# Kernel optimization log

Measured on AMD Instinct MI355X. Metric: run time of the kernel, lower is better.

Reference implementation:

```python
import jax, jax.numpy as jnp
import numpy as np

N_NODES = 100000
N_EDGES = 3200000
N_FEAT = 256
HIDDEN = 64
N_CLASSES = 6


def gcn_conv(x, W, b, src, dst, n_nodes):
    """PyG GCNConv: out = D^{-1/2} (A + I) D^{-1/2} X W + b (self-loops added)."""
    h = x @ W  # [N, out]
    loops = jnp.arange(n_nodes, dtype=src.dtype)
    src2 = jnp.concatenate([src, loops])
    dst2 = jnp.concatenate([dst, loops])
    # degree over destination nodes (edge weight 1), including self-loops
    deg = jax.ops.segment_sum(jnp.ones_like(dst2, dtype=h.dtype), dst2,
                              num_segments=n_nodes)
    dis = jnp.where(deg > 0, jax.lax.rsqrt(deg), 0.0)  # deg^{-1/2}
    norm = dis[src2] * dis[dst2]  # [E+N]
    msg = h[src2] * norm[:, None]  # gather + scale
    out = jax.ops.segment_sum(msg, dst2, num_segments=n_nodes)  # scatter-add
    return out + b


def setup_inputs() -> dict:
    key = jax.random.key(0)
    ks = jax.random.split(key, 5)
    x = jax.random.normal(ks[0], (N_NODES, N_FEAT), dtype=jnp.float32)
    edge_index = jax.random.randint(ks[1], (2, N_EDGES), 0, N_NODES, dtype=jnp.int64)
    W1 = jax.random.normal(ks[2], (N_FEAT, HIDDEN), dtype=jnp.float32) / np.sqrt(N_FEAT)
    b1 = jnp.zeros((HIDDEN,), dtype=jnp.float32)
    W2 = jax.random.normal(ks[3], (HIDDEN, HIDDEN), dtype=jnp.float32) / np.sqrt(HIDDEN)
    b2 = jnp.zeros((HIDDEN,), dtype=jnp.float32)
    Wfc = jax.random.normal(ks[4], (HIDDEN, N_CLASSES), dtype=jnp.float32) / np.sqrt(HIDDEN)
    bfc = jnp.zeros((N_CLASSES,), dtype=jnp.float32)
    return {"x": x, "edge_index": edge_index, "W1": W1, "b1": b1,
            "W2": W2, "b2": b2, "Wfc": Wfc, "bfc": bfc}


def reference(x, edge_index, W1, b1, W2, b2, Wfc, bfc):
    src, dst = edge_index[0], edge_index[1]
    n = x.shape[0]
    h = jax.nn.relu(gcn_conv(x, W1, b1, src, dst, n))
    # dropout(p=0.2) is identity in eval mode
    h = jax.nn.relu(gcn_conv(h, W2, b2, src, dst, n))
    return h @ Wfc + bfc
```

## Files before the change

kernel.cpp:

```cpp
#include <hip/hip_runtime.h>
#include <hip/hip_fp16.h>
#include <math.h>

#define NFEAT 256
#define HID 64
#define NCLS 6
#define NBMX 1600
#define CAPB 4096
#define CHUNK 16384
#define FUSED_LDS 32768

typedef float vf4 __attribute__((ext_vector_type(4)));
typedef int   vi4 __attribute__((ext_vector_type(4)));


__global__ __launch_bounds__(256) void k_count(const int* __restrict__ dst,
                                               int* __restrict__ C, int E, int nbuck) {
  __shared__ int cnt[NBMX];
  int t = threadIdx.x;
  for (int i = t; i < nbuck; i += 256) cnt[i] = 0;
  __syncthreads();
  int e0 = blockIdx.x * CHUNK;
  int e1 = e0 + CHUNK;
  if (e1 > E) e1 = E;
  for (int r0 = e0; r0 < e1; r0 += 1024) {
    int i0 = r0 + t * 4;
    if (i0 + 4 <= e1) {
      vi4 dv = __builtin_nontemporal_load((const vi4*)&dst[i0]);
      atomicAdd(&cnt[dv.x >> 6], 1);
      atomicAdd(&cnt[dv.y >> 6], 1);
      atomicAdd(&cnt[dv.z >> 6], 1);
      atomicAdd(&cnt[dv.w >> 6], 1);
    } else {
      for (int q = 0; q < 4; ++q)
        if (i0 + q < e1) atomicAdd(&cnt[dst[i0 + q] >> 6], 1);
    }
  }
  __syncthreads();
  int* Crow = C + (size_t)blockIdx.x * nbuck;
  for (int i = t; i < nbuck; i += 256) Crow[i] = cnt[i];
}


__global__ __launch_bounds__(256) void k_scan_cols(int* __restrict__ C,
                                                   int* __restrict__ T,
                                                   int nblk, int nbuck) {
  int b = blockIdx.x * 256 + threadIdx.x;
  if (b >= nbuck) return;
  int run = 0;
  int blk = 0;
  for (; blk + 4 <= nblk; blk += 4) {
    int c0 = C[(size_t)(blk + 0) * nbuck + b];
    int c1 = C[(size_t)(blk + 1) * nbuck + b];
    int c2 = C[(size_t)(blk + 2) * nbuck + b];
    int c3 = C[(size_t)(blk + 3) * nbuck + b];
    C[(size_t)(blk + 0) * nbuck + b] = run; run += c0;
    C[(size_t)(blk + 1) * nbuck + b] = run; run += c1;
    C[(size_t)(blk + 2) * nbuck + b] = run; run += c2;
    C[(size_t)(blk + 3) * nbuck + b] = run; run += c3;
  }
  for (; blk < nblk; ++blk) {
    int c = C[(size_t)blk * nbuck + b];
    C[(size_t)blk * nbuck + b] = run;
    run += c;
  }
  T[b] = run;
}


__global__ __launch_bounds__(256) void k_scanb(const int* __restrict__ T,
                                               int* __restrict__ bbase, int nbuck) {
  __shared__ int sh[256];
  __shared__ int carry;
  int t = threadIdx.x;
  if (t == 0) carry = 0;
  __syncthreads();
  for (int base = 0; base < nbuck; base += 256) {
    int v = (base + t < nbuck) ? T[base + t] : 0;
    sh[t] = v;
    __syncthreads();
    for (int off = 1; off < 256; off <<= 1) {
      int x = sh[t];
      int y = (t >= off) ? sh[t - off] : 0;
      __syncthreads();
      sh[t] = x + y;
      __syncthreads();
    }
    if (base + t < nbuck) bbase[base + t] = carry + sh[t] - v;
    __syncthreads();
    if (t == 255) carry += sh[255];
    __syncthreads();
  }
}


__global__ __launch_bounds__(256) void k_fused(const int* __restrict__ src,
                                               const int* __restrict__ dst,
                                               const int* __restrict__ C,
                                               const int* __restrict__ bbase,
                                               unsigned* __restrict__ packed,
                                               int E, int nbuck, int nbb,
                                               const float* __restrict__ X,
                                               const float* __restrict__ W1,
                                               __half* __restrict__ H16, int n) {
  extern __shared__ char smem[];
  int t = threadIdx.x;

  if (blockIdx.x < nbb) {
    int* baseL = (int*)smem;
    int* cnt   = baseL + NBMX;
    const int* Crow = C + (size_t)blockIdx.x * nbuck;
    for (int i = t; i < nbuck; i += 256) {
      baseL[i] = bbase[i] + Crow[i];
      cnt[i] = 0;
    }
    __syncthreads();

    int e0 = blockIdx.x * CHUNK;
    int e1 = e0 + CHUNK;
    if (e1 > E) e1 = E;
    for (int r0 = e0; r0 < e1; r0 += 1024) {
      int i0 = r0 + t * 4;
      int s4[4], d4[4];
      bool full = (i0 + 4 <= e1);
      if (full) {
        vi4 sv = __builtin_nontemporal_load((const vi4*)&src[i0]);
        vi4 dv = __builtin_nontemporal_load((const vi4*)&dst[i0]);
        s4[0] = sv.x; s4[1] = sv.y; s4[2] = sv.z; s4[3] = sv.w;
        d4[0] = dv.x; d4[1] = dv.y; d4[2] = dv.z; d4[3] = dv.w;
      } else {
        for (int q = 0; q < 4; ++q)
          if (i0 + q < e1) { s4[q] = src[i0 + q]; d4[q] = dst[i0 + q]; }
      }
#pragma unroll
      for (int q = 0; q < 4; ++q) {
        if (i0 + q < e1) {
          int b = d4[q] >> 6;
          int slot = atomicAdd(&cnt[b], 1);
          packed[(size_t)baseL[b] + slot] =
              ((unsigned)s4[q] << 6) | (unsigned)(d4[q] & 63);
        }
      }
    }
  } else {
    float* Wl = (float*)smem;
    float* Xl = Wl + 4096;
    const int row0 = (blockIdx.x - nbb) * 64;
    const int tc = t & 15;
    const int tr = t >> 4;
    float acc[4][4] = {};

    for (int k0 = 0; k0 < NFEAT; k0 += 64) {
      __syncthreads();
#pragma unroll
      for (int i = 0; i < 4; ++i) {
        int idx = t * 4 + i * 1024;
        int kr = idx >> 6, c = idx & 63;
        *(vf4*)&Wl[idx] = *(const vf4*)&W1[(size_t)(k0 + kr) * 64 + c];
      }
#pragma unroll
      for (int i = 0; i < 4; ++i) {
        int idx = t * 4 + i * 1024;
        int r = idx >> 6, c = idx & 63;
        int row = row0 + r;
        vf4 v = {0.f, 0.f, 0.f, 0.f};
        if (row < n) v = __builtin_nontemporal_load((const vf4*)&X[(size_t)row * NFEAT + k0 + c]);
        *(vf4*)&Xl[idx] = v;
      }
      __syncthreads();
#pragma unroll 4
      for (int kk = 0; kk < 64; kk += 4) {
        float4 xv[4], wv[4];
#pragma unroll
        for (int r = 0; r < 4; ++r) xv[r] = *(float4*)&Xl[(tr * 4 + r) * 64 + kk];
#pragma unroll
        for (int q = 0; q < 4; ++q) wv[q] = *(float4*)&Wl[(kk + q) * 64 + tc * 4];
#pragma unroll
        for (int r = 0; r < 4; ++r) {
          const float xr[4] = {xv[r].x, xv[r].y, xv[r].z, xv[r].w};
#pragma unroll
          for (int q = 0; q < 4; ++q) {
            acc[r][0] += xr[q] * wv[q].x;
            acc[r][1] += xr[q] * wv[q].y;
            acc[r][2] += xr[q] * wv[q].z;
            acc[r][3] += xr[q] * wv[q].w;
          }
        }
      }
    }
#pragma unroll
    for (int r = 0; r < 4; ++r) {
      int row = row0 + tr * 4 + r;
      if (row < n) {
        __half2 h01 = __floats2half2_rn(acc[r][0], acc[r][1]);
        __half2 h23 = __floats2half2_rn(acc[r][2], acc[r][3]);
        uint2 st;
        st.x = *reinterpret_cast<unsigned*>(&h01);
        st.y = *reinterpret_cast<unsigned*>(&h23);
        ((uint2*)H16)[(size_t)row * 16 + tc] = st;
      }
    }
  }
}


__global__ __launch_bounds__(256) void k_build(unsigned* __restrict__ packed,
                                               const int* __restrict__ T,
                                               const int* __restrict__ bbase,
                                               int2* __restrict__ rowrange,
                                               float* __restrict__ dis,
                                               int n, int nbuck) {
  __shared__ unsigned buf[CAPB];
  __shared__ unsigned outb[CAPB];
  __shared__ int cnt4[4][64];
  __shared__ int cur4[4][64];
  __shared__ int offi[64];
  __shared__ int offx[64];
  __shared__ int cntl[64];
  int b = blockIdx.x;
  int t = threadIdx.x;
  int g = t >> 6;
  int m = T[b];
  if (m > CAPB) m = CAPB;
  int bb = bbase[b];
  unsigned* pb = packed + bb;

  cnt4[g][t & 63] = 0;
  for (int k = t; k < m; k += 256) buf[k] = pb[k];
  __syncthreads();
  for (int k = t; k < m; k += 256) atomicAdd(&cnt4[g][buf[k] & 63u], 1);
  __syncthreads();
  if (t < 64) {
    int c0 = cnt4[0][t], c1 = cnt4[1][t], c2 = cnt4[2][t], c3 = cnt4[3][t];
    int tot = c0 + c1 + c2 + c3;
    cntl[t] = tot;
    offi[t] = tot;
    cur4[0][t] = 0;
    cur4[1][t] = c0;
    cur4[2][t] = c0 + c1;
    cur4[3][t] = c0 + c1 + c2;
  }
  __syncthreads();
  for (int off = 1; off < 64; off <<= 1) {
    int x = (t < 64) ? offi[t] : 0;
    int y = (t >= off && t < 64) ? offi[t - off] : 0;
    __syncthreads();
    if (t < 64) offi[t] = x + y;
    __syncthreads();
  }
  if (t < 64) {
    offx[t] = offi[t] - cntl[t];
    int v = b * 64 + t;
    if (v < n) {
      rowrange[v] = make_int2(bb + offx[t], cntl[t]);
      dis[v] = rsqrtf((float)cntl[t] + 1.0f);
    }
#pragma unroll
    for (int gg = 0; gg < 4; ++gg) cur4[gg][t] += offx[t];
  }
  __syncthreads();
  for (int k = t; k < m; k += 256) {
    unsigned e = buf[k];
    int dl = e & 63u;
    int q = atomicAdd(&cur4[g][dl], 1);
    outb[q] = e >> 6;
  }
  __syncthreads();
  for (int k = t; k < m; k += 256) pb[k] = outb[k];
}


__global__ __launch_bounds__(256) void k_agg_gemm(const int2* __restrict__ rowrange,
                                                  const int* __restrict__ srcs,
                                                  const __half* __restrict__ g16,
                                                  const float* __restrict__ dis,
                                                  const float* __restrict__ b1,
                                                  const float* __restrict__ W2,
                                                  __half* __restrict__ g2out, int n) {
  __shared__ __half2 W2h[64 * 32];
  __shared__ float arow[16][68];
  int t = threadIdx.x;
  for (int i = t; i < 2048; i += 256) {
    float2 f = *(const float2*)&W2[(size_t)i * 2];
    W2h[i] = __floats2half2_rn(f.x, f.y);
  }

  int grp = t >> 4, lane = t & 15;
  int v = blockIdx.x * 16 + grp;
  bool active = (v < n);
  const uint2* g2 = (const uint2*)g16;

  float rx = 0.f, ry = 0.f, rz = 0.f, rw = 0.f;
  if (active) {
    int2 rr = rowrange[v];
    int j = rr.x, end = rr.x + rr.y;
    float dv = dis[v];
    uint2 su = g2[(size_t)v * 16 + lane];
    float2 f0 = __half22float2(*reinterpret_cast<__half2*>(&su.x));
    float2 f1 = __half22float2(*reinterpret_cast<__half2*>(&su.y));
    float ax = dv * f0.x, ay = dv * f0.y, az = dv * f1.x, aw = dv * f1.y;

    for (; j + 8 <= end; j += 8) {
      int s[8];
#pragma unroll
      for (int q = 0; q < 8; ++q) s[q] = __builtin_nontemporal_load(&srcs[j + q]);
      float ds[8];
      uint2 a[8];
#pragma unroll
      for (int q = 0; q < 8; ++q) { ds[q] = dis[s[q]]; a[q] = g2[(size_t)s[q] * 16 + lane]; }
#pragma unroll
      for (int q = 0; q < 8; ++q) {
        float2 p0 = __half22float2(*reinterpret_cast<__half2*>(&a[q].x));
        float2 p1 = __half22float2(*reinterpret_cast<__half2*>(&a[q].y));
        ax = fmaf(ds[q], p0.x, ax); ay = fmaf(ds[q], p0.y, ay);
        az = fmaf(ds[q], p1.x, az); aw = fmaf(ds[q], p1.y, aw);
      }
    }
    for (; j < end; ++j) {
      int s0 = __builtin_nontemporal_load(&srcs[j]);
      float ds = dis[s0];
      uint2 a0 = g2[(size_t)s0 * 16 + lane];
      float2 p0 = __half22float2(*reinterpret_cast<__half2*>(&a0.x));
      float2 p1 = __half22float2(*reinterpret_cast<__half2*>(&a0.y));
      ax = fmaf(ds, p0.x, ax); ay = fmaf(ds, p0.y, ay);
      az = fmaf(ds, p1.x, az); aw = fmaf(ds, p1.y, aw);
    }
    float4 bb = *(const float4*)&b1[lane * 4];
    rx = fmaxf(fmaf(dv, ax, bb.x), 0.f);
    ry = fmaxf(fmaf(dv, ay, bb.y), 0.f);
    rz = fmaxf(fmaf(dv, az, bb.z), 0.f);
    rw = fmaxf(fmaf(dv, aw, bb.w), 0.f);
  }
  arow[grp][lane * 4 + 0] = rx;
  arow[grp][lane * 4 + 1] = ry;
  arow[grp][lane * 4 + 2] = rz;
  arow[grp][lane * 4 + 3] = rw;
  __syncthreads();

  if (active) {
    float o0 = 0.f, o1 = 0.f, o2 = 0.f, o3 = 0.f;
    int c2 = lane * 2;
#pragma unroll 4
    for (int k = 0; k < 64; ++k) {
      float a = arow[grp][k];
      float2 w01 = __half22float2(W2h[k * 32 + c2]);
      float2 w23 = __half22float2(W2h[k * 32 + c2 + 1]);
      o0 = fmaf(a, w01.x, o0);
      o1 = fmaf(a, w01.y, o1);
      o2 = fmaf(a, w23.x, o2);
      o3 = fmaf(a, w23.y, o3);
    }
    float dvv = dis[v];
    __half2 h01 = __floats2half2_rn(o0 * dvv, o1 * dvv);
    __half2 h23 = __floats2half2_rn(o2 * dvv, o3 * dvv);
    uint2 st;
    st.x = *reinterpret_cast<unsigned*>(&h01);
    st.y = *reinterpret_cast<unsigned*>(&h23);
    ((uint2*)g2out)[(size_t)v * 16 + lane] = st;
  }
}


__global__ __launch_bounds__(256) void k_agg_fc(const int2* __restrict__ rowrange,
                                                const int* __restrict__ srcs,
                                                const __half* __restrict__ g16,
                                                const float* __restrict__ dis,
                                                const float* __restrict__ b2,
                                                const float* __restrict__ Wfc,
                                                const float* __restrict__ bfc,
                                                float* __restrict__ outp, int n) {
  __shared__ float Wl[64 * NCLS];
  __shared__ float bl[8];
  int t = threadIdx.x;
  for (int i = t; i < 64 * NCLS; i += 256) Wl[i] = Wfc[i];
  if (t < NCLS) bl[t] = bfc[t];
  __syncthreads();

  int grp = t >> 4, lane = t & 15;
  int v = blockIdx.x * 16 + grp;
  bool active = (v < n);
  const uint2* g2 = (const uint2*)g16;

  float r0 = 0.f, r1 = 0.f, r2 = 0.f, r3 = 0.f;
  if (active) {
    int2 rr = rowrange[v];
    int j = rr.x, end = rr.x + rr.y;
    uint2 su = g2[(size_t)v * 16 + lane];
    float2 f0 = __half22float2(*reinterpret_cast<__half2*>(&su.x));
    float2 f1 = __half22float2(*reinterpret_cast<__half2*>(&su.y));
    float ax = f0.x, ay = f0.y, az = f1.x, aw = f1.y;

    for (; j + 8 <= end; j += 8) {
      int s[8];
#pragma unroll
      for (int q = 0; q < 8; ++q) s[q] = __builtin_nontemporal_load(&srcs[j + q]);
      uint2 a[8];
#pragma unroll
      for (int q = 0; q < 8; ++q) a[q] = g2[(size_t)s[q] * 16 + lane];
#pragma unroll
      for (int q = 0; q < 8; ++q) {
        float2 p0 = __half22float2(*reinterpret_cast<__half2*>(&a[q].x));
        float2 p1 = __half22float2(*reinterpret_cast<__half2*>(&a[q].y));
        ax += p0.x; ay += p0.y; az += p1.x; aw += p1.y;
      }
    }
    for (; j < end; ++j) {
      int s0 = __builtin_nontemporal_load(&srcs[j]);
      uint2 a0 = g2[(size_t)s0 * 16 + lane];
      float2 p0 = __half22float2(*reinterpret_cast<__half2*>(&a0.x));
      float2 p1 = __half22float2(*reinterpret_cast<__half2*>(&a0.y));
      ax += p0.x; ay += p0.y; az += p1.x; aw += p1.y;
    }
    float dv = dis[v];
    float4 bb = *(const float4*)&b2[lane * 4];
    r0 = fmaxf(fmaf(dv, ax, bb.x), 0.f);
    r1 = fmaxf(fmaf(dv, ay, bb.y), 0.f);
    r2 = fmaxf(fmaf(dv, az, bb.z), 0.f);
    r3 = fmaxf(fmaf(dv, aw, bb.w), 0.f);
  }

  float p[NCLS];
#pragma unroll
  for (int jj = 0; jj < NCLS; ++jj) p[jj] = 0.f;
  int k0 = lane * 4;
#pragma unroll
  for (int q = 0; q < 4; ++q) {
    float a = (q == 0) ? r0 : (q == 1) ? r1 : (q == 2) ? r2 : r3;
#pragma unroll
    for (int jj = 0; jj < NCLS; ++jj)
      p[jj] = fmaf(a, Wl[(k0 + q) * NCLS + jj], p[jj]);
  }
#pragma unroll
  for (int m = 1; m < 16; m <<= 1) {
#pragma unroll
    for (int jj = 0; jj < NCLS; ++jj)
      p[jj] += __shfl_xor(p[jj], m, 64);
  }
  if (active && lane < NCLS)
    outp[(size_t)v * NCLS + lane] = p[lane] + bl[lane];
}


extern "C" void kernel_launch(void* const* d_in, const int* in_sizes, int n_in,
                              void* d_out, int out_size, void* d_ws, size_t ws_size,
                              hipStream_t stream) {
  const float* x   = (const float*)d_in[0];
  const int*   ei  = (const int*)d_in[1];
  const float* W1  = (const float*)d_in[2];
  const float* b1  = (const float*)d_in[3];
  const float* W2  = (const float*)d_in[4];
  const float* b2  = (const float*)d_in[5];
  const float* Wfc = (const float*)d_in[6];
  const float* bfc = (const float*)d_in[7];
  float* out = (float*)d_out;

  const int n = in_sizes[0] / NFEAT;
  const int E = in_sizes[1] / 2;
  const int* src = ei;
  const int* dst = ei + E;
  const int nbuck = (n + 63) >> 6;
  const int nbb = (E + CHUNK - 1) / CHUNK;
  const int ntile = (n + 63) / 64;

  char* ws = (char*)d_ws;
  size_t off = 0;
  auto alloc = [&](size_t bytes) -> void* {
    void* p = (void*)(ws + off);
    off += (bytes + 255) & ~(size_t)255;
    return p;
  };
  float* dis      = (float*)alloc((size_t)n * 4);
  int2*  rowrange = (int2*)alloc((size_t)n * 8);
  int*   C        = (int*)alloc((size_t)nbb * nbuck * 4);
  int*   T        = (int*)alloc((size_t)nbuck * 4);
  int*   bbase    = (int*)alloc((size_t)nbuck * 4);
  unsigned* packed = (unsigned*)alloc((size_t)E * 4);
  __half* bufA16  = (__half*)alloc((size_t)n * HID * 2);
  __half* bufC16  = (__half*)alloc((size_t)n * HID * 2);

  k_count<<<nbb, 256, 0, stream>>>(dst, C, E, nbuck);
  k_scan_cols<<<(nbuck + 255) / 256, 256, 0, stream>>>(C, T, nbb, nbuck);
  k_scanb<<<1, 256, 0, stream>>>(T, bbase, nbuck);
  k_fused<<<nbb + ntile, 256, FUSED_LDS, stream>>>(src, dst, C, bbase, packed,
                                                   E, nbuck, nbb, x, W1, bufA16, n);
  k_build<<<nbuck, 256, 0, stream>>>(packed, T, bbase, rowrange, dis, n, nbuck);

  k_agg_gemm<<<(n + 15) / 16, 256, 0, stream>>>(rowrange, (const int*)packed, bufA16,
                                                dis, b1, W2, bufC16, n);

  k_agg_fc<<<(n + 15) / 16, 256, 0, stream>>>(rowrange, (const int*)packed, bufC16,
                                              dis, b2, Wfc, bfc, out, n);
}
```

Before: 288.8 us.

## Prescale layer-1 features by source norm in build; shuffle-based layer-2 GEMM

```diff
diff --git a/kernel.cpp b/kernel.cpp
--- a/kernel.cpp
+++ b/kernel.cpp
@@ -209,6 +209,7 @@
                                                const int* __restrict__ bbase,
                                                int2* __restrict__ rowrange,
                                                float* __restrict__ dis,
+                                               __half* __restrict__ g1,
                                                int n, int nbuck) {
   __shared__ unsigned buf[CAPB];
   __shared__ unsigned outb[CAPB];
@@ -217,6 +218,7 @@
   __shared__ int offi[64];
   __shared__ int offx[64];
   __shared__ int cntl[64];
+  __shared__ float disl[64];
   int b = blockIdx.x;
   int t = threadIdx.x;
   int g = t >> 6;
@@ -250,10 +252,12 @@
   }
   if (t < 64) {
     offx[t] = offi[t] - cntl[t];
+    float dv = rsqrtf((float)cntl[t] + 1.0f);
+    disl[t] = dv;
     int v = b * 64 + t;
     if (v < n) {
       rowrange[v] = make_int2(bb + offx[t], cntl[t]);
-      dis[v] = rsqrtf((float)cntl[t] + 1.0f);
+      dis[v] = dv;
     }
 #pragma unroll
     for (int gg = 0; gg < 4; ++gg) cur4[gg][t] += offx[t];
@@ -267,6 +271,20 @@
   }
   __syncthreads();
   for (int k = t; k < m; k += 256) pb[k] = outb[k];
+
+  __half2* g1h = (__half2*)g1;
+#pragma unroll
+  for (int i = 0; i < 8; ++i) {
+    int idx = t + i * 256;
+    int r = idx >> 5, e = idx & 31;
+    int v = b * 64 + r;
+    if (v < n) {
+      size_t p = (size_t)v * 32 + e;
+      float2 f = __half22float2(g1h[p]);
+      float d = disl[r];
+      g1h[p] = __floats2half2_rn(f.x * d, f.y * d);
+    }
+  }
 }
 
 
@@ -278,86 +296,81 @@
                                                   const float* __restrict__ W2,
                                                   __half* __restrict__ g2out, int n) {
   __shared__ __half2 W2h[64 * 32];
-  __shared__ float arow[16][68];
   int t = threadIdx.x;
   for (int i = t; i < 2048; i += 256) {
     float2 f = *(const float2*)&W2[(size_t)i * 2];
     W2h[i] = __floats2half2_rn(f.x, f.y);
   }
+  __syncthreads();
 
   int grp = t >> 4, lane = t & 15;
   int v = blockIdx.x * 16 + grp;
-  bool active = (v < n);
+  if (v >= n) return;
   const uint2* g2 = (const uint2*)g16;
 
-  float rx = 0.f, ry = 0.f, rz = 0.f, rw = 0.f;
-  if (active) {
-    int2 rr = rowrange[v];
-    int j = rr.x, end = rr.x + rr.y;
-    float dv = dis[v];
-    uint2 su = g2[(size_t)v * 16 + lane];
-    float2 f0 = __half22float2(*reinterpret_cast<__half2*>(&su.x));
-    float2 f1 = __half22float2(*reinterpret_cast<__half2*>(&su.y));
-    float ax = dv * f0.x, ay = dv * f0.y, az = dv * f1.x, aw = dv * f1.y;
-
-    for (; j + 8 <= end; j += 8) {
-      int s[8];
-#pragma unroll
-      for (int q = 0; q < 8; ++q) s[q] = __builtin_nontemporal_load(&srcs[j + q]);
-      float ds[8];
-      uint2 a[8];
-#pragma unroll
-      for (int q = 0; q < 8; ++q) { ds[q] = dis[s[q]]; a[q] = g2[(size_t)s[q] * 16 + lane]; }
-#pragma unroll
-      for (int q = 0; q < 8; ++q) {
-        float2 p0 = __half22float2(*reinterpret_cast<__half2*>(&a[q].x));
-        float2 p1 = __half22float2(*reinterpret_cast<__half2*>(&a[q].y));
-        ax = fmaf(ds[q], p0.x, ax); ay = fmaf(ds[q], p0.y, ay);
-        az = fmaf(ds[q], p1.x, az); aw = fmaf(ds[q], p1.y, aw);
-      }
-    }
-    for (; j < end; ++j) {
-      int s0 = __builtin_nontemporal_load(&srcs[j]);
-      float ds = dis[s0];
-      uint2 a0 = g2[(size_t)s0 * 16 + lane];
-      float2 p0 = __half22float2(*reinterpret_cast<__half2*>(&a0.x));
-      float2 p1 = __half22float2(*reinterpret_cast<__half2*>(&a0.y));
-      ax = fmaf(ds, p0.x, ax); ay = fmaf(ds, p0.y, ay);
-      az = fmaf(ds, p1.x, az); aw = fmaf(ds, p1.y, aw);
-    }
-    float4 bb = *(const float4*)&b1[lane * 4];
-    rx = fmaxf(fmaf(dv, ax, bb.x), 0.f);
-    ry = fmaxf(fmaf(dv, ay, bb.y), 0.f);
-    rz = fmaxf(fmaf(dv, az, bb.z), 0.f);
-    rw = fmaxf(fmaf(dv, aw, bb.w), 0.f);
-  }
-  arow[grp][lane * 4 + 0] = rx;
-  arow[grp][lane * 4 + 1] = ry;
-  arow[grp][lane * 4 + 2] = rz;
-  arow[grp][lane * 4 + 3] = rw;
-  __syncthreads();
-
-  if (active) {
-    float o0 = 0.f, o1 = 0.f, o2 = 0.f, o3 = 0.f;
-    int c2 = lane * 2;
-#pragma unroll 4
-    for (int k = 0; k < 64; ++k) {
-      float a = arow[grp][k];
-      float2 w01 = __half22float2(W2h[k * 32 + c2]);
-      float2 w23 = __half22float2(W2h[k * 32 + c2 + 1]);
-      o0 = fmaf(a, w01.x, o0);
-      o1 = fmaf(a, w01.y, o1);
-      o2 = fmaf(a, w23.x, o2);
-      o3 = fmaf(a, w23.y, o3);
-    }
-    float dvv = dis[v];
-    __half2 h01 = __floats2half2_rn(o0 * dvv, o1 * dvv);
-    __half2 h23 = __floats2half2_rn(o2 * dvv, o3 * dvv);
-    uint2 st;
-    st.x = *reinterpret_cast<unsigned*>(&h01);
-    st.y = *reinterpret_cast<unsigned*>(&h23);
-    ((uint2*)g2out)[(size_t)v * 16 + lane] = st;
-  }
+  int2 rr = rowrange[v];
+  int j = rr.x, end = rr.x + rr.y;
+  uint2 su = g2[(size_t)v * 16 + lane];
+  float2 f0 = __half22float2(*reinterpret_cast<__half2*>(&su.x));
+  float2 f1 = __half22float2(*reinterpret_cast<__half2*>(&su.y));
+  float ax = f0.x, ay = f0.y, az = f1.x, aw = f1.y;
+
+  for (; j + 8 <= end; j += 8) {
+    int s[8];
+#pragma unroll
+    for (int q = 0; q < 8; ++q) s[q] = __builtin_nontemporal_load(&srcs[j + q]);
+    uint2 a[8];
+#pragma unroll
+    for (int q = 0; q < 8; ++q) a[q] = g2[(size_t)s[q] * 16 + lane];
+#pragma unroll
+    for (int q = 0; q < 8; ++q) {
+      float2 p0 = __half22float2(*reinterpret_cast<__half2*>(&a[q].x));
+      float2 p1 = __half22float2(*reinterpret_cast<__half2*>(&a[q].y));
+      ax += p0.x; ay += p0.y; az += p1.x; aw += p1.y;
+    }
+  }
+  for (; j < end; ++j) {
+    int s0 = __builtin_nontemporal_load(&srcs[j]);
+    uint2 a0 = g2[(size_t)s0 * 16 + lane];
+    float2 p0 = __half22float2(*reinterpret_cast<__half2*>(&a0.x));
+    float2 p1 = __half22float2(*reinterpret_cast<__half2*>(&a0.y));
+    ax += p0.x; ay += p0.y; az += p1.x; aw += p1.y;
+  }
+
+  float dv = dis[v];
+  float4 bb = *(const float4*)&b1[lane * 4];
+  float r0 = fmaxf(fmaf(dv, ax, bb.x), 0.f);
+  float r1 = fmaxf(fmaf(dv, ay, bb.y), 0.f);
+  float r2 = fmaxf(fmaf(dv, az, bb.z), 0.f);
+  float r3 = fmaxf(fmaf(dv, aw, bb.w), 0.f);
+
+  float o0 = 0.f, o1 = 0.f, o2 = 0.f, o3 = 0.f;
+  int gbase = (t & 63) & 48;
+  int c2 = lane * 2;
+#pragma unroll
+  for (int kk = 0; kk < 16; ++kk) {
+    int sl = gbase + kk;
+    float a0 = __shfl(r0, sl, 64);
+    float a1 = __shfl(r1, sl, 64);
+    float a2 = __shfl(r2, sl, 64);
+    float a3 = __shfl(r3, sl, 64);
+    int k = kk * 4;
+    float2 w;
+    w = __half22float2(W2h[(k + 0) * 32 + c2]);     o0 = fmaf(a0, w.x, o0); o1 = fmaf(a0, w.y, o1);
+    w = __half22float2(W2h[(k + 0) * 32 + c2 + 1]); o2 = fmaf(a0, w.x, o2); o3 = fmaf(a0, w.y, o3);
+    w = __half22float2(W2h[(k + 1) * 32 + c2]);     o0 = fmaf(a1, w.x, o0); o1 = fmaf(a1, w.y, o1);
+    w = __half22float2(W2h[(k + 1) * 32 + c2 + 1]); o2 = fmaf(a1, w.x, o2); o3 = fmaf(a1, w.y, o3);
+    w = __half22float2(W2h[(k + 2) * 32 + c2]);     o0 = fmaf(a2, w.x, o0); o1 = fmaf(a2, w.y, o1);
+    w = __half22float2(W2h[(k + 2) * 32 + c2 + 1]); o2 = fmaf(a2, w.x, o2); o3 = fmaf(a2, w.y, o3);
+    w = __half22float2(W2h[(k + 3) * 32 + c2]);     o0 = fmaf(a3, w.x, o0); o1 = fmaf(a3, w.y, o1);
+    w = __half22float2(W2h[(k + 3) * 32 + c2 + 1]); o2 = fmaf(a3, w.x, o2); o3 = fmaf(a3, w.y, o3);
+  }
+  __half2 h01 = __floats2half2_rn(o0 * dv, o1 * dv);
+  __half2 h23 = __floats2half2_rn(o2 * dv, o3 * dv);
+  uint2 st;
+  st.x = *reinterpret_cast<unsigned*>(&h01);
+  st.y = *reinterpret_cast<unsigned*>(&h23);
+  ((uint2*)g2out)[(size_t)v * 16 + lane] = st;
 }
 
 
@@ -483,7 +496,7 @@
   k_scanb<<<1, 256, 0, stream>>>(T, bbase, nbuck);
   k_fused<<<nbb + ntile, 256, FUSED_LDS, stream>>>(src, dst, C, bbase, packed,
                                                    E, nbuck, nbb, x, W1, bufA16, n);
-  k_build<<<nbuck, 256, 0, stream>>>(packed, T, bbase, rowrange, dis, n, nbuck);
+  k_build<<<nbuck, 256, 0, stream>>>(packed, T, bbase, rowrange, dis, bufA16, n, nbuck);
 
   k_agg_gemm<<<(n + 15) / 16, 256, 0, stream>>>(rowrange, (const int*)packed, bufA16,
                                                 dis, b1, W2, bufC16, n);
```

Result: no change. 285.5 us (-1.1%).
